# Optimization experiments

Measured on AMD Instinct MI355X. Metric: run time of the kernel, lower is better.

Reference implementation:

```python
import jax, jax.numpy as jnp
import numpy as np

T, N, D = 4096, 128, 128
NEG = -1.0e9


def setup_inputs() -> dict:
    key = jax.random.key(0)
    k1, k2, k3, k4 = jax.random.split(key, 4)
    return {
        "query": jax.random.normal(k1, (N, D), dtype=jnp.float32),
        "key": jax.random.normal(k2, (T, N, D), dtype=jnp.float32),
        "value": jax.random.normal(k3, (T, N, D), dtype=jnp.float32),
        "lens_for_attention": jax.random.randint(k4, (N,), 1, T + 1, dtype=jnp.int64 if jax.config.jax_enable_x64 else jnp.int32),
    }


def reference(query, key, value, lens_for_attention):
    # key, value: (T, N, D) -> (N, T, D)
    k = jnp.transpose(key, (1, 0, 2))
    v = jnp.transpose(value, (1, 0, 2))
    t = k.shape[1]
    # mask: True where timestep index >= length (padded positions)
    mask = jnp.arange(t)[None, :] >= lens_for_attention[:, None]  # (N, T)
    # energy = bmm(key, query): (N, T, D) @ (N, D) -> (N, T)
    energy = jnp.einsum('ntd,nd->nt', k, query)
    energy = jnp.where(mask, NEG, energy)
    attention = jax.nn.softmax(energy, axis=1)  # (N, T)
    # context = bmm(attention, value): (N, T) @ (N, T, D) -> (N, D)
    out = jnp.einsum('nt,ntd->nd', attention, v)
    return (out, attention)
```

## Files before the change

### kernel.cpp

```cpp
#include <hip/hip_runtime.h>

#define T_DIM 4096
#define N_DIM 128
#define D_DIM 128
#define CHUNK 256
#define NCHUNK (T_DIM / CHUNK)
#define NEGE (-1.0e9f)

__global__ __launch_bounds__(256) void energy_kernel(
    const float* __restrict__ q,
    const float* __restrict__ key,
    const int*   __restrict__ lens,
    float*       __restrict__ att,
    float*       __restrict__ blockmax)
{
    const int b    = blockIdx.x;
    const int n    = b & (N_DIM - 1);
    const int c    = b >> 7;
    const int t0   = c * CHUNK;
    const int len  = lens[n];
    const int tid  = threadIdx.x;

    if (t0 >= len) {
        att[(size_t)n * T_DIM + t0 + tid] = NEGE;
        if (tid == 0) blockmax[n * NCHUNK + c] = NEGE;
        return;
    }

    const int wave = tid >> 6;
    const int lane = tid & 63;
    const int half = lane >> 5;
    const int l32  = lane & 31;

    const float4 qv = *(const float4*)(q + n * D_DIM + l32 * 4);

    float lmax = NEGE;

    #pragma unroll 4
    for (int i = 0; i < CHUNK / 8; ++i) {
        const int t = t0 + wave * 2 + i * 8 + half;
        float e;
        if (t < len) {
            const float4 kv = *(const float4*)(key + (size_t)t * (N_DIM * D_DIM)
                                               + n * D_DIM + l32 * 4);
            float p = kv.x * qv.x + kv.y * qv.y + kv.z * qv.z + kv.w * qv.w;
            p += __shfl_xor(p, 1);
            p += __shfl_xor(p, 2);
            p += __shfl_xor(p, 4);
            p += __shfl_xor(p, 8);
            p += __shfl_xor(p, 16);
            e = p;
        } else {
            e = NEGE;
        }
        if (l32 == 0) att[(size_t)n * T_DIM + t] = e;
        lmax = fmaxf(lmax, e);
    }

    lmax = fmaxf(lmax, __shfl_xor(lmax, 32));
    __shared__ float smax[4];
    if (lane == 0) smax[wave] = lmax;
    __syncthreads();
    if (tid == 0) {
        blockmax[n * NCHUNK + c] =
            fmaxf(fmaxf(smax[0], smax[1]), fmaxf(smax[2], smax[3]));
    }
}

__global__ __launch_bounds__(256) void softmax_kernel(
    float* __restrict__ att,
    const float* __restrict__ blockmax)
{
    const int n   = blockIdx.x;
    const int tid = threadIdx.x;
    const int wave = tid >> 6;
    const int lane = tid & 63;

    __shared__ float sm;
    __shared__ float ssum[4];
    __shared__ float stot;

    if (tid == 0) {
        float m = blockmax[n * NCHUNK];
        #pragma unroll
        for (int i = 1; i < NCHUNK; ++i) m = fmaxf(m, blockmax[n * NCHUNK + i]);
        sm = m;
    }
    __syncthreads();
    const float m = sm;

    float4* row = (float4*)(att + (size_t)n * T_DIM);
    float4 vals[4];
    float sum = 0.f;
    #pragma unroll
    for (int i = 0; i < 4; ++i) {
        float4 v = row[tid + i * 256];
        v.x = __expf(v.x - m);
        v.y = __expf(v.y - m);
        v.z = __expf(v.z - m);
        v.w = __expf(v.w - m);
        sum += v.x + v.y + v.z + v.w;
        vals[i] = v;
    }
    sum += __shfl_xor(sum, 1);
    sum += __shfl_xor(sum, 2);
    sum += __shfl_xor(sum, 4);
    sum += __shfl_xor(sum, 8);
    sum += __shfl_xor(sum, 16);
    sum += __shfl_xor(sum, 32);
    if (lane == 0) ssum[wave] = sum;
    __syncthreads();
    if (tid == 0) stot = ssum[0] + ssum[1] + ssum[2] + ssum[3];
    __syncthreads();
    const float inv = 1.0f / stot;

    #pragma unroll
    for (int i = 0; i < 4; ++i) {
        float4 v = vals[i];
        v.x *= inv; v.y *= inv; v.z *= inv; v.w *= inv;
        row[tid + i * 256] = v;
    }
}

__global__ __launch_bounds__(256) void pv_kernel(
    const float* __restrict__ att,
    const float* __restrict__ value,
    const int*   __restrict__ lens,
    float*       __restrict__ partial)
{
    const int b    = blockIdx.x;
    const int n    = b & (N_DIM - 1);
    const int c    = b >> 7;
    const int t0   = c * CHUNK;
    const int len  = lens[n];
    const int tid  = threadIdx.x;
    const int d    = tid & (D_DIM - 1);
    const int half = tid >> 7;

    if (t0 >= len) {
        if (tid < D_DIM)
            partial[((size_t)n * NCHUNK + c) * D_DIM + tid] = 0.0f;
        return;
    }

    const int tend = min(t0 + CHUNK, len);
    float acc = 0.f;
    #pragma unroll 4
    for (int t = t0 + half; t < tend; t += 2) {
        const float a = att[(size_t)n * T_DIM + t];
        acc += a * value[(size_t)t * (N_DIM * D_DIM) + n * D_DIM + d];
    }

    __shared__ float buf[256];
    buf[tid] = acc;
    __syncthreads();
    if (tid < D_DIM) {
        partial[((size_t)n * NCHUNK + c) * D_DIM + tid] =
            buf[tid] + buf[tid + D_DIM];
    }
}

__global__ __launch_bounds__(256) void reduce_kernel(
    const float* __restrict__ partial,
    float*       __restrict__ out)
{
    const int idx = blockIdx.x * 256 + threadIdx.x;
    const int n = idx >> 7;
    const int d = idx & (D_DIM - 1);
    float s = 0.f;
    #pragma unroll
    for (int c = 0; c < NCHUNK; ++c)
        s += partial[((size_t)n * NCHUNK + c) * D_DIM + d];
    out[idx] = s;
}

extern "C" void kernel_launch(void* const* d_in, const int* in_sizes, int n_in,
                              void* d_out, int out_size, void* d_ws, size_t ws_size,
                              hipStream_t stream) {
    const float* q     = (const float*)d_in[0];
    const float* key   = (const float*)d_in[1];
    const float* value = (const float*)d_in[2];
    const int*   lens  = (const int*)d_in[3];

    float* out = (float*)d_out;
    float* att = out + N_DIM * D_DIM;

    float* blockmax = (float*)d_ws;
    float* partial  = (float*)((char*)d_ws + 8192);

    energy_kernel <<<N_DIM * NCHUNK, 256, 0, stream>>>(q, key, lens, att, blockmax);
    softmax_kernel<<<N_DIM,          256, 0, stream>>>(att, blockmax);
    pv_kernel     <<<N_DIM * NCHUNK, 256, 0, stream>>>(att, value, lens, partial);
    reduce_kernel <<<(N_DIM * D_DIM) / 256, 256, 0, stream>>>(partial, out);
}
```

Before: 483.8 us.

## Fuse PV partial reduction via atomics and vectorize value loads

Result: no change. 479.9 us (-0.8%).

```diff
diff --git a/kernel.cpp b/kernel.cpp
--- a/kernel.cpp
+++ b/kernel.cpp
@@ -69,25 +69,24 @@
 
 __global__ __launch_bounds__(256) void softmax_kernel(
     float* __restrict__ att,
-    const float* __restrict__ blockmax)
+    const float* __restrict__ blockmax,
+    float* __restrict__ out)
 {
     const int n   = blockIdx.x;
     const int tid = threadIdx.x;
     const int wave = tid >> 6;
     const int lane = tid & 63;
 
-    __shared__ float sm;
+    __shared__ float smaxarr[NCHUNK];
     __shared__ float ssum[4];
     __shared__ float stot;
 
-    if (tid == 0) {
-        float m = blockmax[n * NCHUNK];
-        #pragma unroll
-        for (int i = 1; i < NCHUNK; ++i) m = fmaxf(m, blockmax[n * NCHUNK + i]);
-        sm = m;
-    }
+    if (tid < NCHUNK) smaxarr[tid] = blockmax[n * NCHUNK + tid];
+    if (tid < 32) ((float4*)(out + n * D_DIM))[tid] = make_float4(0.f, 0.f, 0.f, 0.f);
     __syncthreads();
-    const float m = sm;
+    float m = smaxarr[0];
+    #pragma unroll
+    for (int i = 1; i < NCHUNK; ++i) m = fmaxf(m, smaxarr[i]);
 
     float4* row = (float4*)(att + (size_t)n * T_DIM);
     float4 vals[4];
@@ -126,52 +125,55 @@
     const float* __restrict__ att,
     const float* __restrict__ value,
     const int*   __restrict__ lens,
-    float*       __restrict__ partial)
+    float*       __restrict__ out)
 {
     const int b    = blockIdx.x;
     const int n    = b & (N_DIM - 1);
     const int c    = b >> 7;
     const int t0   = c * CHUNK;
     const int len  = lens[n];
+
+    if (t0 >= len) return;
+
     const int tid  = threadIdx.x;
-    const int d    = tid & (D_DIM - 1);
-    const int half = tid >> 7;
+    const int qd   = tid & 31;
+    const int g    = tid >> 5;
+    const int tend = min(t0 + CHUNK, len);
 
-    if (t0 >= len) {
-        if (tid < D_DIM)
-            partial[((size_t)n * NCHUNK + c) * D_DIM + tid] = 0.0f;
-        return;
+    float4 acc = make_float4(0.f, 0.f, 0.f, 0.f);
+    #pragma unroll 4
+    for (int t = t0 + g; t < tend; t += 8) {
+        const float a = att[(size_t)n * T_DIM + t];
+        const float4 v = *(const float4*)(value + (size_t)t * (N_DIM * D_DIM)
+                                          + n * D_DIM + qd * 4);
+        acc.x += a * v.x;
+        acc.y += a * v.y;
+        acc.z += a * v.z;
+        acc.w += a * v.w;
     }
 
-    const int tend = min(t0 + CHUNK, len);
-    float acc = 0.f;
-    #pragma unroll 4
-    for (int t = t0 + half; t < tend; t += 2) {
-        const float a = att[(size_t)n * T_DIM + t];
-        acc += a * value[(size_t)t * (N_DIM * D_DIM) + n * D_DIM + d];
-    }
-
-    __shared__ float buf[256];
+    __shared__ float4 buf[256];
     buf[tid] = acc;
     __syncthreads();
-    if (tid < D_DIM) {
-        partial[((size_t)n * NCHUNK + c) * D_DIM + tid] =
-            buf[tid] + buf[tid + D_DIM];
+    if (tid < 128) {
+        float4 o = buf[tid + 128];
+        buf[tid].x += o.x; buf[tid].y += o.y; buf[tid].z += o.z; buf[tid].w += o.w;
     }
-}
-
-__global__ __launch_bounds__(256) void reduce_kernel(
-    const float* __restrict__ partial,
-    float*       __restrict__ out)
-{
-    const int idx = blockIdx.x * 256 + threadIdx.x;
-    const int n = idx >> 7;
-    const int d = idx & (D_DIM - 1);
-    float s = 0.f;
-    #pragma unroll
-    for (int c = 0; c < NCHUNK; ++c)
-        s += partial[((size_t)n * NCHUNK + c) * D_DIM + d];
-    out[idx] = s;
+    __syncthreads();
+    if (tid < 64) {
+        float4 o = buf[tid + 64];
+        buf[tid].x += o.x; buf[tid].y += o.y; buf[tid].z += o.z; buf[tid].w += o.w;
+    }
+    __syncthreads();
+    if (tid < 32) {
+        float4 a0 = buf[tid];
+        float4 a1 = buf[tid + 32];
+        float* dst = out + n * D_DIM + tid * 4;
+        atomicAdd(dst + 0, a0.x + a1.x);
+        atomicAdd(dst + 1, a0.y + a1.y);
+        atomicAdd(dst + 2, a0.z + a1.z);
+        atomicAdd(dst + 3, a0.w + a1.w);
+    }
 }
 
 extern "C" void kernel_launch(void* const* d_in, const int* in_sizes, int n_in,
@@ -186,10 +188,8 @@
     float* att = out + N_DIM * D_DIM;
 
     float* blockmax = (float*)d_ws;
-    float* partial  = (float*)((char*)d_ws + 8192);
 
     energy_kernel <<<N_DIM * NCHUNK, 256, 0, stream>>>(q, key, lens, att, blockmax);
-    softmax_kernel<<<N_DIM,          256, 0, stream>>>(att, blockmax);
-    pv_kernel     <<<N_DIM * NCHUNK, 256, 0, stream>>>(att, value, lens, partial);
-    reduce_kernel <<<(N_DIM * D_DIM) / 256, 256, 0, stream>>>(partial, out);
+    softmax_kernel<<<N_DIM,          256, 0, stream>>>(att, blockmax, out);
+    pv_kernel     <<<N_DIM * NCHUNK, 256, 0, stream>>>(att, value, lens, out);
 }
```
